# Kernel optimization log

Hardware: AMD Instinct MI355X
Metric: run time of the kernel (lower is better)

Reference implementation:

```python
import jax, jax.numpy as jnp
import numpy as np
from jax.ops import segment_sum

N = 20000; IN = 256; HID = 256; Z = 64; DEC_H = 64; E = 120000; NEG = 5
BETA = 1.0; LN_EPS = 1e-5; TAU_MIN = 1e-4


def setup_inputs() -> dict:
    rng = np.random.default_rng(0)
    a = rng.integers(0, N, E)
    b = (a + 1 + rng.integers(0, N - 1, E)) % N  # guarantees a != b
    lo, hi = np.minimum(a, b), np.maximum(a, b)
    pos_edge = jnp.asarray(np.stack([lo, hi]), dtype=jnp.int32)          # [2,E], i<j single copy
    edge_index = jnp.asarray(np.stack([np.concatenate([lo, hi]),
                                       np.concatenate([hi, lo])]), dtype=jnp.int32)  # [2,2E] undirected
    neg_edge = jnp.asarray(rng.integers(0, N, (2, NEG * E)), dtype=jnp.int32)
    ks = jax.random.split(jax.random.key(0), 12)
    p = lambda i, shape, s=0.02: (jax.random.normal(ks[i], shape, jnp.float32) * s)
    return dict(
        x=p(0, (N, IN), 1.0), eps=p(1, (N, Z), 1.0),
        edge_index=edge_index, pos_edge=pos_edge, neg_edge=neg_edge,
        W1=p(2, (IN, HID)), b1=jnp.zeros((HID,), jnp.float32),
        g1=jnp.ones((HID,), jnp.float32), bt1=jnp.zeros((HID,), jnp.float32),
        Wmu=p(3, (HID, Z)), bmu=jnp.zeros((Z,), jnp.float32),
        Wlv=p(4, (HID, Z)), blv=jnp.zeros((Z,), jnp.float32),
        Wd1=p(5, (Z, Z)), bd1=jnp.zeros((Z,), jnp.float32),
        Wd2=p(6, (Z, Z)), bd2=jnp.zeros((Z,), jnp.float32),
        Wa=p(7, (4 * Z, DEC_H)), ba=jnp.zeros((DEC_H,), jnp.float32),
        Wb=p(8, (DEC_H, 1)), bb=jnp.zeros((1,), jnp.float32),
        tau=jnp.array(1.0, jnp.float32))


def _gcn_plain(h, src, dst, W, b):
    # GCNConv(add_self_loops=False, normalize=False): unnormalized scatter-add
    m = h @ W                                   # [N,F]
    return segment_sum(m[src], dst, num_segments=N) + b


def _gcn_norm(h, src, dst, W, b):
    # GCNConv defaults: self loops + symmetric normalization
    loops = jnp.arange(N, dtype=src.dtype)
    s = jnp.concatenate([src, loops]); d = jnp.concatenate([dst, loops])
    deg = segment_sum(jnp.ones_like(d, jnp.float32), d, num_segments=N)  # in-degree incl self
    dis = jax.lax.rsqrt(jnp.maximum(deg, 1.0))
    norm = dis[s] * dis[d]                      # [Emsg+N]
    m = h @ W
    return segment_sum(m[s] * norm[:, None], d, num_segments=N) + b


def _layernorm(h, g, bt):
    mu = jnp.mean(h, axis=-1, keepdims=True)
    var = jnp.mean((h - mu) ** 2, axis=-1, keepdims=True)
    return (h - mu) * jax.lax.rsqrt(var + LN_EPS) * g + bt


def _forward(x, eps, edge_index, pos_edge, neg_edge, W1, b1, g1, bt1, Wmu, bmu,
             Wlv, blv, Wd1, bd1, Wd2, bd2, Wa, ba, Wb, bb, tau):
    src, dst = edge_index[0], edge_index[1]
    # Encoder (dropout inactive: eval-mode reference)
    h1 = jax.nn.relu(_layernorm(_gcn_plain(x, src, dst, W1, b1), g1, bt1))
    mu = _gcn_plain(h1, src, dst, Wmu, bmu)
    logvar = _gcn_plain(h1, src, dst, Wlv, blv)
    z = mu + eps * jnp.exp(0.5 * logvar)
    # EdgeDecoder: 2 normalized GCN passes over positive (i<j) edges only
    ps, pd = pos_edge[0], pos_edge[1]
    h = jax.nn.relu(_gcn_norm(z, ps, pd, Wd1, bd1))
    h = jax.nn.relu(_gcn_norm(h, ps, pd, Wd2, bd2))
    # edge gather -> concat features -> MLP
    eu = jnp.concatenate([pos_edge[0], neg_edge[0]])
    ev = jnp.concatenate([pos_edge[1], neg_edge[1]])
    hu, hv = h[eu], h[ev]                        # [Ep+En, Z]
    phi = jnp.concatenate([hu, hv, jnp.abs(hu - hv), hu * hv], axis=-1)  # [Ep+En, 4Z]
    logits = (jax.nn.relu(phi @ Wa + ba) @ Wb + bb)[:, 0]
    logits = logits / jnp.clip(tau, TAU_MIN)
    # weighted BCE-with-logits; pos_weight = #neg/#pos = NEG
    n_pos = pos_edge.shape[1]; n_neg = neg_edge.shape[1]
    labels = jnp.concatenate([jnp.ones((n_pos,), jnp.float32), jnp.zeros((n_neg,), jnp.float32)])
    pw = jnp.float32(n_neg) / jnp.float32(n_pos)
    recon = -jnp.mean(pw * labels * jax.nn.log_sigmoid(logits)
                      + (1.0 - labels) * jax.nn.log_sigmoid(-logits))
    kl = -0.5 * jnp.mean(1.0 + logvar - mu ** 2 - jnp.exp(logvar))
    loss = recon + BETA * kl
    return loss, recon, kl


def reference(x, eps, edge_index, pos_edge, neg_edge, W1, b1, g1, bt1, Wmu, bmu,
              Wlv, blv, Wd1, bd1, Wd2, bd2, Wa, ba, Wb, bb, tau):
    return _forward(x, eps, edge_index, pos_edge, neg_edge, W1, b1, g1, bt1, Wmu,
                    bmu, Wlv, blv, Wd1, bd1, Wd2, bd2, Wa, ba, Wb, bb, tau)
```

## Files before the change

kernel.cpp:

```cpp
#include <hip/hip_runtime.h>
#include <hip/hip_bf16.h>
#include <hip/hip_fp16.h>
#include <math.h>

#define N_NODES 20000
#define E2      240000
#define EP      120000
#define ENEG    600000
#define ETOT    720000
#define NTILE   11250
#define POSTILE 1875
#define EMLP_BLOCKS 1024
#define NCHUNK  20

#define WA_B  64
#define W1T_B 256
#define WML_B 128
#define UV_B  2813
#define HA_B  938
#define HP_B  469
#define FA_B  938
#define FP_B  469
#define DIS_B 79

typedef __attribute__((ext_vector_type(8))) short bf16x8;
typedef __attribute__((ext_vector_type(8))) _Float16 f16x8;
typedef __attribute__((ext_vector_type(4))) float f32x4;

__device__ __forceinline__ float logsigf(float x) {
    return fminf(x, 0.0f) - log1pf(expf(-fabsf(x)));
}

__device__ __forceinline__ unsigned short f2bf(float f) {
    unsigned u = __float_as_uint(f);
    u += 0x7FFF + ((u >> 16) & 1);
    return (unsigned short)(u >> 16);
}

__device__ __forceinline__ unsigned short f2h(float f) {
    return __half_as_ushort(__float2half(f));
}

__device__ __forceinline__ float bflo(unsigned u) { return __uint_as_float(u << 16); }
__device__ __forceinline__ float bfhi(unsigned u) { return __uint_as_float(u & 0xFFFF0000u); }

__device__ __forceinline__ void store_out(float v, float* p) { *p = v; }
__device__ __forceinline__ void store_out(float v, unsigned short* p) { *p = f2bf(v); }
__device__ __forceinline__ void store_out(float v, __half* p) { *p = __float2half(v); }
__device__ __forceinline__ float load_in(const float* p) { return *p; }
__device__ __forceinline__ float load_in(const unsigned short* p) {
    return __uint_as_float(((unsigned)*p) << 16);
}
__device__ __forceinline__ float load_in(const __half* p) { return __half2float(*p); }

union I4H { int4 i; __half2 h[4]; f16x8 f; };

__device__ __forceinline__ f16x8 make_ad16(int4 a, int4 b) {
    I4H ua, ub, r;
    ua.i = a; ub.i = b;
#pragma unroll
    for (int k = 0; k < 4; ++k) r.h[k] = __habs2(__hsub2(ua.h[k], ub.h[k]));
    return r.f;
}

__device__ __forceinline__ f16x8 make_pr16(int4 a, int4 b) {
    I4H ua, ub, r;
    ua.i = a; ub.i = b;
#pragma unroll
    for (int k = 0; k < 4; ++k) r.h[k] = __hmul2(ua.h[k], ub.h[k]);
    return r.f;
}

__global__ void k_prep_csr(const float* __restrict__ Wa, unsigned short* __restrict__ WaT,
                           const float* __restrict__ W1, unsigned short* __restrict__ W1T,
                           const float* __restrict__ Wmu, const float* __restrict__ Wlv,
                           unsigned short* __restrict__ WmlT,
                           const int* __restrict__ pos, const int* __restrict__ neg,
                           int2* __restrict__ uv,
                           const int* __restrict__ e_dst, int* __restrict__ cntA,
                           const int* __restrict__ pd, int* __restrict__ cntP) {
    const int b = blockIdx.x, tid = threadIdx.x;
    if (b < WA_B) {
        const int idx = b * 256 + tid;
        const int n = idx >> 8, kp = idx & 255;
        const int part = kp >> 6;
        const int d = ((kp >> 3) & 3) * 16 + ((kp >> 5) & 1) * 8 + (kp & 7);
        WaT[idx] = f2h(Wa[(part * 64 + d) * 64 + n]);
    } else if (b < WA_B + W1T_B) {
        const int idx = (b - WA_B) * 256 + tid;
        const int n = idx >> 8, k = idx & 255;
        W1T[idx] = f2bf(W1[k * 256 + n]);
    } else if (b < WA_B + W1T_B + WML_B) {
        const int idx = (b - WA_B - W1T_B) * 256 + tid;
        const int n = idx >> 8, k = idx & 255;
        const float* W = (n & 1) ? Wlv : Wmu;
        WmlT[idx] = f2bf(W[k * 64 + (n >> 1)]);
    } else if (b < WA_B + W1T_B + WML_B + UV_B) {
        const int j = (b - WA_B - W1T_B - WML_B) * 256 + tid;
        if (j < ETOT) {
            int u, v;
            if (j < EP) { u = pos[j]; v = pos[EP + j]; }
            else        { u = neg[j - EP]; v = neg[ENEG + (j - EP)]; }
            uv[j] = make_int2(u, v);
        }
    } else if (b < WA_B + W1T_B + WML_B + UV_B + HA_B) {
        const int e = (b - WA_B - W1T_B - WML_B - UV_B) * 256 + tid;
        if (e < E2) atomicAdd(&cntA[e_dst[e]], 1);
    } else {
        const int e = (b - WA_B - W1T_B - WML_B - UV_B - HA_B) * 256 + tid;
        if (e < EP) atomicAdd(&cntP[pd[e]], 1);
    }
}

__global__ __launch_bounds__(1024) void k_scan_par(const int* __restrict__ cntA,
                                                   int* __restrict__ rsA,
                                                   int* __restrict__ curA,
                                                   const int* __restrict__ cntP,
                                                   int* __restrict__ rsP,
                                                   int* __restrict__ curP) {
    const int arr = blockIdx.x / NCHUNK;
    const int c   = blockIdx.x % NCHUNK;
    const int* cnt = arr ? cntP : cntA;
    int* rs  = arr ? rsP  : rsA;
    int* cur = arr ? curP : curA;
    const int tid = threadIdx.x, lane = tid & 63, wid = tid >> 6;
    __shared__ int wred[16];

    int p = 0;
    for (int i = tid; i < c * 1024; i += 1024) p += cnt[i];
    for (int o = 32; o > 0; o >>= 1) p += __shfl_xor(p, o, 64);
    if (lane == 0) wred[wid] = p;
    __syncthreads();
    int prefix = 0;
#pragma unroll
    for (int k = 0; k < 16; ++k) prefix += wred[k];
    __syncthreads();

    const int i = c * 1024 + tid;
    const int v = (i < N_NODES) ? cnt[i] : 0;
    int x = v;
#pragma unroll
    for (int d = 1; d < 64; d <<= 1) {
        const int t = __shfl_up(x, d, 64);
        if (lane >= d) x += t;
    }
    if (lane == 63) wred[wid] = x;
    __syncthreads();
    int wexc = 0, tot = 0;
#pragma unroll
    for (int k = 0; k < 16; ++k) { if (k < wid) wexc += wred[k]; tot += wred[k]; }
    const int excl = prefix + wexc + x - v;
    if (i < N_NODES) { rs[i] = excl; cur[i] = excl; }
    if (c == NCHUNK - 1 && tid == 0) rs[N_NODES] = prefix + tot;
}

__global__ void k_finish_csr(const int* __restrict__ e_src, const int* __restrict__ e_dst,
                             int* __restrict__ curA, int* __restrict__ adjA,
                             const int* __restrict__ ps, const int* __restrict__ pd,
                             int* __restrict__ curP, int* __restrict__ adjP,
                             const int* __restrict__ rsP, float* __restrict__ dis) {
    const int b = blockIdx.x, tid = threadIdx.x;
    if (b < FA_B) {
        const int e = b * 256 + tid;
        if (e < E2) {
            const int p = atomicAdd(&curA[e_dst[e]], 1);
            adjA[p] = e_src[e];
        }
    } else if (b < FA_B + FP_B) {
        const int e = (b - FA_B) * 256 + tid;
        if (e < EP) {
            const int p = atomicAdd(&curP[pd[e]], 1);
            adjP[p] = ps[e];
        }
    } else {
        const int i = (b - FA_B - FP_B) * 256 + tid;
        if (i < N_NODES) dis[i] = rsqrtf((float)(rsP[i + 1] - rsP[i] + 1));
    }
}

__global__ __launch_bounds__(256) void k_mm_xW1_mfma(const float* __restrict__ x,
                                                     const unsigned short* __restrict__ W1T,
                                                     unsigned short* __restrict__ m1) {
    __shared__ unsigned short sA[32 * 264];
    const int tid = threadIdx.x;
    const int w = tid >> 6, lane = tid & 63;
    const int l15 = lane & 15, quad = lane >> 4;
    const int mb = blockIdx.x >> 2, nb = blockIdx.x & 3;

    for (int i = tid; i < 2048; i += 256) {
        const int row = i >> 6, kc = (i & 63) << 2;
        const float4 xv = *(const float4*)&x[((long)mb * 32 + row) * 256 + kc];
        union { unsigned short s[4]; unsigned long long ll; } pk;
        pk.s[0] = f2bf(xv.x); pk.s[1] = f2bf(xv.y);
        pk.s[2] = f2bf(xv.z); pk.s[3] = f2bf(xv.w);
        *(unsigned long long*)&sA[row * 264 + kc] = pk.ll;
    }

    bf16x8 breg[8];
#pragma unroll
    for (int ks = 0; ks < 8; ++ks)
        breg[ks] = *(const bf16x8*)&W1T[((nb * 64 + w * 16 + l15) << 8) + ks * 32 + quad * 8];
    __syncthreads();

    f32x4 acc[2];
    acc[0] = (f32x4){0.f,0.f,0.f,0.f};
    acc[1] = (f32x4){0.f,0.f,0.f,0.f};
#pragma unroll
    for (int ks = 0; ks < 8; ++ks) {
#pragma unroll
        for (int st = 0; st < 2; ++st) {
            const bf16x8 af = *(const bf16x8*)&sA[(st * 16 + l15) * 264 + ks * 32 + quad * 8];
            acc[st] = __builtin_amdgcn_mfma_f32_16x16x32_bf16(af, breg[ks], acc[st], 0, 0, 0);
        }
    }
#pragma unroll
    for (int st = 0; st < 2; ++st)
#pragma unroll
        for (int r = 0; r < 4; ++r)
            m1[((long)mb * 32 + st * 16 + quad * 4 + r) * 256 + nb * 64 + w * 16 + l15] =
                f2bf(acc[st][r]);
}

__global__ __launch_bounds__(256) void k_gather_ln(const unsigned short* __restrict__ m1,
                                                   const int* __restrict__ rs,
                                                   const int* __restrict__ adj,
                                                   const float* __restrict__ b1,
                                                   const float* __restrict__ g1,
                                                   const float* __restrict__ bt1,
                                                   unsigned short* __restrict__ h1) {
    const int wid = threadIdx.x >> 6, lane = threadIdx.x & 63;
    const int n = blockIdx.x * 4 + wid;
    const int beg = rs[n], end = rs[n + 1];
    float4 a0 = {0.f,0.f,0.f,0.f}, a1 = {0.f,0.f,0.f,0.f};
    float4 a2 = {0.f,0.f,0.f,0.f}, a3 = {0.f,0.f,0.f,0.f};
    int j = beg;
    for (; j + 3 < end; j += 4) {
        const int s0 = adj[j], s1 = adj[j + 1], s2 = adj[j + 2], s3 = adj[j + 3];
        const uint2 u0 = *(const uint2*)(m1 + (long)s0 * 256 + lane * 4);
        const uint2 u1 = *(const uint2*)(m1 + (long)s1 * 256 + lane * 4);
        const uint2 u2 = *(const uint2*)(m1 + (long)s2 * 256 + lane * 4);
        const uint2 u3 = *(const uint2*)(m1 + (long)s3 * 256 + lane * 4);
        a0.x += bflo(u0.x); a0.y += bfhi(u0.x); a0.z += bflo(u0.y); a0.w += bfhi(u0.y);
        a1.x += bflo(u1.x); a1.y += bfhi(u1.x); a1.z += bflo(u1.y); a1.w += bfhi(u1.y);
        a2.x += bflo(u2.x); a2.y += bfhi(u2.x); a2.z += bflo(u2.y); a2.w += bfhi(u2.y);
        a3.x += bflo(u3.x); a3.y += bfhi(u3.x); a3.z += bflo(u3.y); a3.w += bfhi(u3.y);
    }
    for (; j < end; ++j) {
        const int s0 = adj[j];
        const uint2 u = *(const uint2*)(m1 + (long)s0 * 256 + lane * 4);
        a0.x += bflo(u.x); a0.y += bfhi(u.x); a0.z += bflo(u.y); a0.w += bfhi(u.y);
    }
    float4 v;
    const float4 b = *(const float4*)(b1 + lane * 4);
    v.x = (a0.x + a1.x) + (a2.x + a3.x) + b.x;
    v.y = (a0.y + a1.y) + (a2.y + a3.y) + b.y;
    v.z = (a0.z + a1.z) + (a2.z + a3.z) + b.z;
    v.w = (a0.w + a1.w) + (a2.w + a3.w) + b.w;
    float s  = v.x + v.y + v.z + v.w;
    float sq = v.x * v.x + v.y * v.y + v.z * v.z + v.w * v.w;
    for (int o = 32; o > 0; o >>= 1) {
        s  += __shfl_xor(s, o, 64);
        sq += __shfl_xor(sq, o, 64);
    }
    const float mean = s * (1.0f / 256.0f);
    const float var  = sq * (1.0f / 256.0f) - mean * mean;
    const float rsv = rsqrtf(var + 1e-5f);
    const float4 g  = *(const float4*)(g1 + lane * 4);
    const float4 bt = *(const float4*)(bt1 + lane * 4);
    union { unsigned short sh[4]; unsigned long long ll; } pk;
    pk.sh[0] = f2bf(fmaxf((v.x - mean) * rsv * g.x + bt.x, 0.f));
    pk.sh[1] = f2bf(fmaxf((v.y - mean) * rsv * g.y + bt.y, 0.f));
    pk.sh[2] = f2bf(fmaxf((v.z - mean) * rsv * g.z + bt.z, 0.f));
    pk.sh[3] = f2bf(fmaxf((v.w - mean) * rsv * g.w + bt.w, 0.f));
    *(unsigned long long*)&h1[(long)n * 256 + lane * 4] = pk.ll;
}

__global__ __launch_bounds__(256) void k_mm_hml_mfma(const unsigned short* __restrict__ h1,
                                                     const unsigned short* __restrict__ WmlT,
                                                     unsigned short* __restrict__ hml) {
    __shared__ unsigned short sA[32 * 264];
    const int tid = threadIdx.x;
    const int w = tid >> 6, lane = tid & 63;
    const int l15 = lane & 15, quad = lane >> 4;
    const int mb = blockIdx.x >> 1, nb = blockIdx.x & 1;

    for (int i = tid; i < 1024; i += 256) {
        const int row = i >> 5, kc = (i & 31) << 3;
        *(int4*)&sA[row * 264 + kc] = *(const int4*)&h1[((long)mb * 32 + row) * 256 + kc];
    }

    bf16x8 breg[8];
#pragma unroll
    for (int ks = 0; ks < 8; ++ks)
        breg[ks] = *(const bf16x8*)&WmlT[((nb * 64 + w * 16 + l15) << 8) + ks * 32 + quad * 8];
    __syncthreads();

    f32x4 acc[2];
    acc[0] = (f32x4){0.f,0.f,0.f,0.f};
    acc[1] = (f32x4){0.f,0.f,0.f,0.f};
#pragma unroll
    for (int ks = 0; ks < 8; ++ks) {
#pragma unroll
        for (int st = 0; st < 2; ++st) {
            const bf16x8 af = *(const bf16x8*)&sA[(st * 16 + l15) * 264 + ks * 32 + quad * 8];
            acc[st] = __builtin_amdgcn_mfma_f32_16x16x32_bf16(af, breg[ks], acc[st], 0, 0, 0);
        }
    }
#pragma unroll
    for (int st = 0; st < 2; ++st)
#pragma unroll
        for (int r = 0; r < 4; ++r)
            hml[((long)mb * 32 + st * 16 + quad * 4 + r) * 128 + nb * 64 + w * 16 + l15] =
                f2bf(acc[st][r]);
}

__global__ __launch_bounds__(256) void k_gather_mulv(const unsigned short* __restrict__ hml,
                                                     const int* __restrict__ rs,
                                                     const int* __restrict__ adj,
                                                     const float* __restrict__ bmu,
                                                     const float* __restrict__ blv,
                                                     const float* __restrict__ eps,
                                                     unsigned short* __restrict__ z,
                                                     double* __restrict__ kl_part) {
    __shared__ double sKL[4];
    const int wid = threadIdx.x >> 6, lane = threadIdx.x & 63;
    const int n = blockIdx.x * 4 + wid;
    const int beg = rs[n], end = rs[n + 1];
    float m0 = 0.f, m1_ = 0.f, m2 = 0.f, m3 = 0.f;
    float l0 = 0.f, l1 = 0.f, l2 = 0.f, l3 = 0.f;
    int j = beg;
    for (; j + 3 < end; j += 4) {
        const int s0 = adj[j], s1 = adj[j + 1], s2 = adj[j + 2], s3 = adj[j + 3];
        const unsigned u0 = *(const unsigned*)(hml + (long)s0 * 128 + lane * 2);
        const unsigned u1 = *(const unsigned*)(hml + (long)s1 * 128 + lane * 2);
        const unsigned u2 = *(const unsigned*)(hml + (long)s2 * 128 + lane * 2);
        const unsigned u3 = *(const unsigned*)(hml + (long)s3 * 128 + lane * 2);
        m0 += bflo(u0); l0 += bfhi(u0);
        m1_ += bflo(u1); l1 += bfhi(u1);
        m2 += bflo(u2); l2 += bfhi(u2);
        m3 += bflo(u3); l3 += bfhi(u3);
    }
    for (; j < end; ++j) {
        const int s0 = adj[j];
        const unsigned u0 = *(const unsigned*)(hml + (long)s0 * 128 + lane * 2);
        m0 += bflo(u0); l0 += bfhi(u0);
    }
    const float mu = (m0 + m1_) + (m2 + m3) + bmu[lane];
    const float lv = (l0 + l1) + (l2 + l3) + blv[lane];
    z[(long)n * 64 + lane] = f2bf(mu + eps[(long)n * 64 + lane] * expf(0.5f * lv));
    float term = 1.0f + lv - mu * mu - expf(lv);
    for (int o = 32; o > 0; o >>= 1) term += __shfl_xor(term, o, 64);
    if (lane == 0) sKL[wid] = (double)term;
    __syncthreads();
    if (threadIdx.x == 0)
        kl_part[blockIdx.x] = sKL[0] + sKL[1] + sKL[2] + sKL[3];
}

template <typename IN, typename OUT>
__global__ __launch_bounds__(256) void k_dec_fused(const IN* __restrict__ feat,
                                                   const int* __restrict__ rs,
                                                   const int* __restrict__ adj,
                                                   const float* __restrict__ dis,
                                                   const float* __restrict__ Wd,
                                                   const float* __restrict__ bd,
                                                   OUT* __restrict__ out) {
    __shared__ float sW[64 * 64];
    __shared__ float rows[4][64];
    const int tid = threadIdx.x;
    {
        const float4* w4 = (const float4*)Wd;
        float4* sw4 = (float4*)sW;
        for (int i = tid; i < 1024; i += 256) sw4[i] = w4[i];
    }
    const int wid = tid >> 6, lane = tid & 63;
    const int n = blockIdx.x * 4 + wid;
    const int beg = rs[n], end = rs[n + 1];
    float a0 = 0.f, a1 = 0.f, a2 = 0.f, a3 = 0.f;
    int j = beg;
    for (; j + 3 < end; j += 4) {
        const int s0 = adj[j], s1 = adj[j + 1], s2 = adj[j + 2], s3 = adj[j + 3];
        a0 += load_in(&feat[(long)s0 * 64 + lane]) * dis[s0];
        a1 += load_in(&feat[(long)s1 * 64 + lane]) * dis[s1];
        a2 += load_in(&feat[(long)s2 * 64 + lane]) * dis[s2];
        a3 += load_in(&feat[(long)s3 * 64 + lane]) * dis[s3];
    }
    for (; j < end; ++j) {
        const int s0 = adj[j];
        a0 += load_in(&feat[(long)s0 * 64 + lane]) * dis[s0];
    }
    const float dn = dis[n];
    rows[wid][lane] = ((a0 + a1) + (a2 + a3)) * dn
                    + load_in(&feat[(long)n * 64 + lane]) * dn * dn;
    __syncthreads();
    float acc = 0.f;
    for (int k = 0; k < 64; k += 4) {
        const float4 a = *(const float4*)&rows[wid][k];
        acc += a.x * sW[(k+0)*64+lane] + a.y * sW[(k+1)*64+lane]
             + a.z * sW[(k+2)*64+lane] + a.w * sW[(k+3)*64+lane];
    }
    store_out(fmaxf(acc + bd[lane], 0.f), &out[(long)n * 64 + lane]);
}

__global__ __launch_bounds__(256, 2) void k_edge_mlp_mfma(
        const __half* __restrict__ h2,
        const int2* __restrict__ uv,
        const unsigned short* __restrict__ WaT,
        const float* __restrict__ ba,
        const float* __restrict__ Wb,
        const float* __restrict__ bb,
        const float* __restrict__ tau,
        double* __restrict__ recon_part) {
    __shared__ double sRed[4];
    const int tid = threadIdx.x;
    const int w = tid >> 6, lane = tid & 63;
    const int l15 = lane & 15, quad = lane >> 4;

    f16x8 areg[4][8];
#pragma unroll
    for (int nt = 0; nt < 4; ++nt)
#pragma unroll
        for (int ks = 0; ks < 8; ++ks)
            areg[nt][ks] = *(const f16x8*)&WaT[((nt * 16 + l15) << 8) + ks * 32 + quad * 8];

    const float bb0 = bb[0];
    const float itau = 1.0f / fmaxf(tau[0], 1e-4f);

    float lsum = 0.f;

    int t = blockIdx.x;
    int2 uvp = uv[t * 64 + w * 16 + l15];
    int4 hua = *(const int4*)(h2 + (long)uvp.x * 64 + quad * 16);
    int4 hub = *(const int4*)(h2 + (long)uvp.x * 64 + quad * 16 + 8);
    int4 hva = *(const int4*)(h2 + (long)uvp.y * 64 + quad * 16);
    int4 hvb = *(const int4*)(h2 + (long)uvp.y * 64 + quad * 16 + 8);

    for (; t < NTILE; t += EMLP_BLOCKS) {
        const int tn = t + EMLP_BLOCKS;
        int2 uvn = uvp;
        if (tn < NTILE) uvn = uv[tn * 64 + w * 16 + l15];

        const f16x8 fad_a = make_ad16(hua, hva);
        const f16x8 fad_b = make_ad16(hub, hvb);
        const f16x8 fpr_a = make_pr16(hua, hva);
        const f16x8 fpr_b = make_pr16(hub, hvb);

        f32x4 acc[4];
#pragma unroll
        for (int nt = 0; nt < 4; ++nt) acc[nt] = (f32x4){0.f, 0.f, 0.f, 0.f};

        const f16x8 bhu_a = *(const f16x8*)&hua;
        const f16x8 bhu_b = *(const f16x8*)&hub;
        const f16x8 bhv_a = *(const f16x8*)&hva;
        const f16x8 bhv_b = *(const f16x8*)&hvb;

#pragma unroll
        for (int nt = 0; nt < 4; ++nt) {
            acc[nt] = __builtin_amdgcn_mfma_f32_16x16x32_f16(areg[nt][0], bhu_a, acc[nt], 0, 0, 0);
            acc[nt] = __builtin_amdgcn_mfma_f32_16x16x32_f16(areg[nt][1], bhu_b, acc[nt], 0, 0, 0);
            acc[nt] = __builtin_amdgcn_mfma_f32_16x16x32_f16(areg[nt][2], bhv_a, acc[nt], 0, 0, 0);
            acc[nt] = __builtin_amdgcn_mfma_f32_16x16x32_f16(areg[nt][3], bhv_b, acc[nt], 0, 0, 0);
            acc[nt] = __builtin_amdgcn_mfma_f32_16x16x32_f16(areg[nt][4], fad_a, acc[nt], 0, 0, 0);
            acc[nt] = __builtin_amdgcn_mfma_f32_16x16x32_f16(areg[nt][5], fad_b, acc[nt], 0, 0, 0);
            acc[nt] = __builtin_amdgcn_mfma_f32_16x16x32_f16(areg[nt][6], fpr_a, acc[nt], 0, 0, 0);
            acc[nt] = __builtin_amdgcn_mfma_f32_16x16x32_f16(areg[nt][7], fpr_b, acc[nt], 0, 0, 0);
        }

        if (tn < NTILE) {
            hua = *(const int4*)(h2 + (long)uvn.x * 64 + quad * 16);
            hub = *(const int4*)(h2 + (long)uvn.x * 64 + quad * 16 + 8);
            hva = *(const int4*)(h2 + (long)uvn.y * 64 + quad * 16);
            hvb = *(const int4*)(h2 + (long)uvn.y * 64 + quad * 16 + 8);
        }
        uvp = uvn;

        float s = 0.f;
#pragma unroll
        for (int nt = 0; nt < 4; ++nt) {
            const float4 b4 = *(const float4*)&ba[nt * 16 + quad * 4];
            const float4 w4 = *(const float4*)&Wb[nt * 16 + quad * 4];
            s += fmaxf(acc[nt][0] + b4.x, 0.f) * w4.x
               + fmaxf(acc[nt][1] + b4.y, 0.f) * w4.y
               + fmaxf(acc[nt][2] + b4.z, 0.f) * w4.z
               + fmaxf(acc[nt][3] + b4.w, 0.f) * w4.w;
        }
        s += __shfl_xor(s, 16, 64);
        s += __shfl_xor(s, 32, 64);
        if (lane < 16) {
            const float logit = (s + bb0) * itau;
            const bool isPos = (t < POSTILE);
            lsum += isPos ? 5.0f * logsigf(logit) : logsigf(-logit);
        }
    }

    for (int o = 32; o > 0; o >>= 1) lsum += __shfl_xor(lsum, o, 64);
    if (lane == 0) sRed[w] = (double)lsum;
    __syncthreads();
    if (tid == 0)
        recon_part[blockIdx.x] = sRed[0] + sRed[1] + sRed[2] + sRed[3];
}

__global__ __launch_bounds__(1024) void k_final(const double* __restrict__ kl_part,
                                                const double* __restrict__ recon_part,
                                                float* __restrict__ out) {
    __shared__ double sK[16], sR[16];
    const int tid = threadIdx.x, lane = tid & 63, wid = tid >> 6;
    double kl = 0.0, rc = 0.0;
    for (int i = tid; i < 5000; i += 1024) kl += kl_part[i];
    for (int i = tid; i < EMLP_BLOCKS; i += 1024) rc += recon_part[i];
    for (int o = 32; o > 0; o >>= 1) {
        kl += __shfl_xor(kl, o, 64);
        rc += __shfl_xor(rc, o, 64);
    }
    if (lane == 0) { sK[wid] = kl; sR[wid] = rc; }
    __syncthreads();
    if (tid == 0) {
        double K = 0.0, R = 0.0;
        for (int i = 0; i < 16; ++i) { K += sK[i]; R += sR[i]; }
        const double recon = -R / (double)ETOT;
        const double klv = -0.5 * K / ((double)N_NODES * 64.0);
        out[0] = (float)(recon + klv);
        out[1] = (float)recon;
        out[2] = (float)klv;
    }
}

extern "C" void kernel_launch(void* const* d_in, const int* in_sizes, int n_in,
                              void* d_out, int out_size, void* d_ws, size_t ws_size,
                              hipStream_t stream) {
    const float* x   = (const float*)d_in[0];
    const float* eps = (const float*)d_in[1];
    const int* EI    = (const int*)d_in[2];
    const int* pos   = (const int*)d_in[3];
    const int* neg   = (const int*)d_in[4];
    const float* W1  = (const float*)d_in[5];
    const float* b1  = (const float*)d_in[6];
    const float* g1  = (const float*)d_in[7];
    const float* bt1 = (const float*)d_in[8];
    const float* Wmu = (const float*)d_in[9];
    const float* bmu = (const float*)d_in[10];
    const float* Wlv = (const float*)d_in[11];
    const float* blv = (const float*)d_in[12];
    const float* Wd1 = (const float*)d_in[13];
    const float* bd1 = (const float*)d_in[14];
    const float* Wd2 = (const float*)d_in[15];
    const float* bd2 = (const float*)d_in[16];
    const float* Wa  = (const float*)d_in[17];
    const float* ba  = (const float*)d_in[18];
    const float* Wb  = (const float*)d_in[19];
    const float* bb  = (const float*)d_in[20];
    const float* tau = (const float*)d_in[21];

    const int* e_src = EI;
    const int* e_dst = EI + E2;
    const int* ps = pos;
    const int* pd = pos + EP;

    float* ws = (float*)d_ws;
    unsigned short* m1bf  = (unsigned short*)ws;
    unsigned short* hmlbf = (unsigned short*)ws;
    __half* hdec = (__half*)(ws + 2560000);
    __half* h2   = (__half*)(ws + 3840000);
    unsigned short* h1bf = (unsigned short*)(ws + 5120000);
    unsigned short* z    = (unsigned short*)(ws + 10240000);
    float* dis   = ws + 11520000;
    unsigned short* WaT = (unsigned short*)(ws + 11540004);
    int* cntA = (int*)(ws + 11548200);
    int* rsA  = (int*)(ws + 11568200);
    int* adjA = (int*)(ws + 11588204);
    int* cntP = (int*)(ws + 11828204);
    int* rsP  = (int*)(ws + 11848204);
    int* adjP = (int*)(ws + 11868208);
    int2* uv  = (int2*)(ws + 11988208);
    double* kl_part    = (double*)(ws + 13428208);
    double* recon_part = (double*)(ws + 13438208);
    unsigned short* W1T  = (unsigned short*)(ws + 13440256);
    unsigned short* WmlT = (unsigned short*)(ws + 13473024);
    int* curA = (int*)(ws + 13489408);
    int* curP = (int*)(ws + 13509408);

    hipMemsetAsync(cntA, 0, N_NODES * 4, stream);
    hipMemsetAsync(cntP, 0, N_NODES * 4, stream);

    k_prep_csr<<<WA_B + W1T_B + WML_B + UV_B + HA_B + HP_B, 256, 0, stream>>>(
        Wa, WaT, W1, W1T, Wmu, Wlv, WmlT, pos, neg, uv, e_dst, cntA, pd, cntP);
    k_scan_par<<<2 * NCHUNK, 1024, 0, stream>>>(cntA, rsA, curA, cntP, rsP, curP);
    k_finish_csr<<<FA_B + FP_B + DIS_B, 256, 0, stream>>>(
        e_src, e_dst, curA, adjA, ps, pd, curP, adjP, rsP, dis);

    k_mm_xW1_mfma<<<2500, 256, 0, stream>>>(x, W1T, m1bf);
    k_gather_ln<<<5000, 256, 0, stream>>>(m1bf, rsA, adjA, b1, g1, bt1, h1bf);
    k_mm_hml_mfma<<<1250, 256, 0, stream>>>(h1bf, WmlT, hmlbf);
    k_gather_mulv<<<5000, 256, 0, stream>>>(hmlbf, rsA, adjA, bmu, blv, eps, z, kl_part);

    k_dec_fused<unsigned short, __half><<<5000, 256, 0, stream>>>(
        z, rsP, adjP, dis, Wd1, bd1, hdec);
    k_dec_fused<__half, __half><<<5000, 256, 0, stream>>>(
        hdec, rsP, adjP, dis, Wd2, bd2, h2);

    k_edge_mlp_mfma<<<EMLP_BLOCKS, 256, 0, stream>>>(h2, uv, WaT, ba, Wb, bb, tau, recon_part);
    k_final<<<1, 1024, 0, stream>>>(kl_part, recon_part, (float*)d_out);
}
```

Before: 319.9 us.

## Fuse final reduction into edge MLP via atomics and deepen gather prefetch

Removes the separate k_final launch. KL partials are now accumulated with double atomicAdd, and the edge-MLP blocks add their recon sums atomically; a last-block counter writes the three outputs. The edge-MLP loop also prefetches node features one tile ahead and edge indices two tiles ahead, so gather latency overlaps the MFMA work. The costs are 5000 double atomics on one address, possible nondeterministic summation order, and extra registers from the deeper prefetch.

```diff
diff --git a/kernel.cpp b/kernel.cpp
--- a/kernel.cpp
+++ b/kernel.cpp
@@ -78,9 +78,15 @@
                            const int* __restrict__ pos, const int* __restrict__ neg,
                            int2* __restrict__ uv,
                            const int* __restrict__ e_dst, int* __restrict__ cntA,
-                           const int* __restrict__ pd, int* __restrict__ cntP) {
+                           const int* __restrict__ pd, int* __restrict__ cntP,
+                           double* __restrict__ ctrl) {
     const int b = blockIdx.x, tid = threadIdx.x;
     if (b < WA_B) {
+        if (b == 0 && tid == 0) {
+            ctrl[0] = 0.0;
+            ctrl[1] = 0.0;
+            ((int*)(ctrl + 2))[0] = 0;
+        }
         const int idx = b * 256 + tid;
         const int n = idx >> 8, kp = idx & 255;
         const int part = kp >> 6;
@@ -321,7 +327,7 @@
                                                      const float* __restrict__ blv,
                                                      const float* __restrict__ eps,
                                                      unsigned short* __restrict__ z,
-                                                     double* __restrict__ kl_part) {
+                                                     double* __restrict__ kl_acc) {
     __shared__ double sKL[4];
     const int wid = threadIdx.x >> 6, lane = threadIdx.x & 63;
     const int n = blockIdx.x * 4 + wid;
@@ -353,7 +359,7 @@
     if (lane == 0) sKL[wid] = (double)term;
     __syncthreads();
     if (threadIdx.x == 0)
-        kl_part[blockIdx.x] = sKL[0] + sKL[1] + sKL[2] + sKL[3];
+        atomicAdd(kl_acc, sKL[0] + sKL[1] + sKL[2] + sKL[3]);
 }
 
 template <typename IN, typename OUT>
@@ -409,7 +415,8 @@
         const float* __restrict__ Wb,
         const float* __restrict__ bb,
         const float* __restrict__ tau,
-        double* __restrict__ recon_part) {
+        double* __restrict__ ctrl,
+        float* __restrict__ out) {
     __shared__ double sRed[4];
     const int tid = threadIdx.x;
     const int w = tid >> 6, lane = tid & 63;
@@ -428,16 +435,24 @@
     float lsum = 0.f;
 
     int t = blockIdx.x;
-    int2 uvp = uv[t * 64 + w * 16 + l15];
-    int4 hua = *(const int4*)(h2 + (long)uvp.x * 64 + quad * 16);
-    int4 hub = *(const int4*)(h2 + (long)uvp.x * 64 + quad * 16 + 8);
-    int4 hva = *(const int4*)(h2 + (long)uvp.y * 64 + quad * 16);
-    int4 hvb = *(const int4*)(h2 + (long)uvp.y * 64 + quad * 16 + 8);
+    const int slot = w * 16 + l15;
+    int2 uvA = uv[t * 64 + slot];
+    int4 hua = *(const int4*)(h2 + (long)uvA.x * 64 + quad * 16);
+    int4 hub = *(const int4*)(h2 + (long)uvA.x * 64 + quad * 16 + 8);
+    int4 hva = *(const int4*)(h2 + (long)uvA.y * 64 + quad * 16);
+    int4 hvb = *(const int4*)(h2 + (long)uvA.y * 64 + quad * 16 + 8);
+    int2 uvB = (t + EMLP_BLOCKS < NTILE) ? uv[(t + EMLP_BLOCKS) * 64 + slot] : uvA;
 
     for (; t < NTILE; t += EMLP_BLOCKS) {
-        const int tn = t + EMLP_BLOCKS;
-        int2 uvn = uvp;
-        if (tn < NTILE) uvn = uv[tn * 64 + w * 16 + l15];
+        const int t2 = t + 2 * EMLP_BLOCKS;
+        const int2 uvC = (t2 < NTILE) ? uv[t2 * 64 + slot] : uvB;
+        int4 nhua = hua, nhub = hub, nhva = hva, nhvb = hvb;
+        if (t + EMLP_BLOCKS < NTILE) {
+            nhua = *(const int4*)(h2 + (long)uvB.x * 64 + quad * 16);
+            nhub = *(const int4*)(h2 + (long)uvB.x * 64 + quad * 16 + 8);
+            nhva = *(const int4*)(h2 + (long)uvB.y * 64 + quad * 16);
+            nhvb = *(const int4*)(h2 + (long)uvB.y * 64 + quad * 16 + 8);
+        }
 
         const f16x8 fad_a = make_ad16(hua, hva);
         const f16x8 fad_b = make_ad16(hub, hvb);
@@ -465,14 +480,6 @@
             acc[nt] = __builtin_amdgcn_mfma_f32_16x16x32_f16(areg[nt][7], fpr_b, acc[nt], 0, 0, 0);
         }
 
-        if (tn < NTILE) {
-            hua = *(const int4*)(h2 + (long)uvn.x * 64 + quad * 16);
-            hub = *(const int4*)(h2 + (long)uvn.x * 64 + quad * 16 + 8);
-            hva = *(const int4*)(h2 + (long)uvn.y * 64 + quad * 16);
-            hvb = *(const int4*)(h2 + (long)uvn.y * 64 + quad * 16 + 8);
-        }
-        uvp = uvn;
-
         float s = 0.f;
 #pragma unroll
         for (int nt = 0; nt < 4; ++nt) {
@@ -487,40 +494,30 @@
         s += __shfl_xor(s, 32, 64);
         if (lane < 16) {
             const float logit = (s + bb0) * itau;
-            const bool isPos = (t < POSTILE);
-            lsum += isPos ? 5.0f * logsigf(logit) : logsigf(-logit);
-        }
+            lsum += (t < POSTILE) ? 5.0f * logsigf(logit) : logsigf(-logit);
+        }
+
+        hua = nhua; hub = nhub; hva = nhva; hvb = nhvb;
+        uvB = uvC;
     }
 
     for (int o = 32; o > 0; o >>= 1) lsum += __shfl_xor(lsum, o, 64);
     if (lane == 0) sRed[w] = (double)lsum;
     __syncthreads();
-    if (tid == 0)
-        recon_part[blockIdx.x] = sRed[0] + sRed[1] + sRed[2] + sRed[3];
-}
-
-__global__ __launch_bounds__(1024) void k_final(const double* __restrict__ kl_part,
-                                                const double* __restrict__ recon_part,
-                                                float* __restrict__ out) {
-    __shared__ double sK[16], sR[16];
-    const int tid = threadIdx.x, lane = tid & 63, wid = tid >> 6;
-    double kl = 0.0, rc = 0.0;
-    for (int i = tid; i < 5000; i += 1024) kl += kl_part[i];
-    for (int i = tid; i < EMLP_BLOCKS; i += 1024) rc += recon_part[i];
-    for (int o = 32; o > 0; o >>= 1) {
-        kl += __shfl_xor(kl, o, 64);
-        rc += __shfl_xor(rc, o, 64);
-    }
-    if (lane == 0) { sK[wid] = kl; sR[wid] = rc; }
-    __syncthreads();
     if (tid == 0) {
-        double K = 0.0, R = 0.0;
-        for (int i = 0; i < 16; ++i) { K += sK[i]; R += sR[i]; }
-        const double recon = -R / (double)ETOT;
-        const double klv = -0.5 * K / ((double)N_NODES * 64.0);
-        out[0] = (float)(recon + klv);
-        out[1] = (float)recon;
-        out[2] = (float)klv;
+        atomicAdd(&ctrl[1], sRed[0] + sRed[1] + sRed[2] + sRed[3]);
+        __threadfence();
+        int* ctr = (int*)(ctrl + 2);
+        const int old = atomicAdd(ctr, 1);
+        if (old == EMLP_BLOCKS - 1) {
+            const double R = atomicAdd(&ctrl[1], 0.0);
+            const double K = ctrl[0];
+            const double recon = -R / (double)ETOT;
+            const double klv = -0.5 * K / ((double)N_NODES * 64.0);
+            out[0] = (float)(recon + klv);
+            out[1] = (float)recon;
+            out[2] = (float)klv;
+        }
     }
 }
 
@@ -571,8 +568,7 @@
     int* rsP  = (int*)(ws + 11848204);
     int* adjP = (int*)(ws + 11868208);
     int2* uv  = (int2*)(ws + 11988208);
-    double* kl_part    = (double*)(ws + 13428208);
-    double* recon_part = (double*)(ws + 13438208);
+    double* ctrl = (double*)(ws + 13428208);
     unsigned short* W1T  = (unsigned short*)(ws + 13440256);
     unsigned short* WmlT = (unsigned short*)(ws + 13473024);
     int* curA = (int*)(ws + 13489408);
@@ -582,7 +578,7 @@
     hipMemsetAsync(cntP, 0, N_NODES * 4, stream);
 
     k_prep_csr<<<WA_B + W1T_B + WML_B + UV_B + HA_B + HP_B, 256, 0, stream>>>(
-        Wa, WaT, W1, W1T, Wmu, Wlv, WmlT, pos, neg, uv, e_dst, cntA, pd, cntP);
+        Wa, WaT, W1, W1T, Wmu, Wlv, WmlT, pos, neg, uv, e_dst, cntA, pd, cntP, ctrl);
     k_scan_par<<<2 * NCHUNK, 1024, 0, stream>>>(cntA, rsA, curA, cntP, rsP, curP);
     k_finish_csr<<<FA_B + FP_B + DIS_B, 256, 0, stream>>>(
         e_src, e_dst, curA, adjA, ps, pd, curP, adjP, rsP, dis);
@@ -590,13 +586,13 @@
     k_mm_xW1_mfma<<<2500, 256, 0, stream>>>(x, W1T, m1bf);
     k_gather_ln<<<5000, 256, 0, stream>>>(m1bf, rsA, adjA, b1, g1, bt1, h1bf);
     k_mm_hml_mfma<<<1250, 256, 0, stream>>>(h1bf, WmlT, hmlbf);
-    k_gather_mulv<<<5000, 256, 0, stream>>>(hmlbf, rsA, adjA, bmu, blv, eps, z, kl_part);
+    k_gather_mulv<<<5000, 256, 0, stream>>>(hmlbf, rsA, adjA, bmu, blv, eps, z, ctrl);
 
     k_dec_fused<unsigned short, __half><<<5000, 256, 0, stream>>>(
         z, rsP, adjP, dis, Wd1, bd1, hdec);
     k_dec_fused<__half, __half><<<5000, 256, 0, stream>>>(
         hdec, rsP, adjP, dis, Wd2, bd2, h2);
 
-    k_edge_mlp_mfma<<<EMLP_BLOCKS, 256, 0, stream>>>(h2, uv, WaT, ba, Wb, bb, tau, recon_part);
-    k_final<<<1, 1024, 0, stream>>>(kl_part, recon_part, (float*)d_out);
-}
+    k_edge_mlp_mfma<<<EMLP_BLOCKS, 256, 0, stream>>>(
+        h2, uv, WaT, ba, Wb, bb, tau, ctrl, (float*)d_out);
+}
```

Result: slower. 390.5 us (+22.1%).
